# Kernel optimization log

Hardware: AMD Instinct MI355X
Metric: run time of the kernel (lower is better)

The kernel has to match this reference:

```python
import math
import jax, jax.numpy as jnp
import numpy as np

SCALING = 16.0 / 32.0  # alpha / rank


def real_fourier_orthogonal_multiply(c):
    """Vectorized equivalent of the per-frequency Python loop: build a complex
    spectrum from real Fourier coefficients and inverse-rfft along last dim."""
    n = c.shape[-1]
    sqrt_n = math.sqrt(n)
    pair_scale = math.sqrt(n / 2.0)
    max_f = (n - 1) // 2
    work = c.astype(jnp.float32)
    dc = (work[..., 0] * sqrt_n)[..., None].astype(jnp.complex64)
    cos = work[..., 1:1 + 2 * max_f:2] * pair_scale
    sin = work[..., 2:2 + 2 * max_f:2] * pair_scale
    mid = (cos - 1j * sin).astype(jnp.complex64)  # freqs 1..max_f
    parts = [dc, mid]
    if n % 2 == 0:
        parts.append((work[..., -1] * sqrt_n)[..., None].astype(jnp.complex64))
    spectrum = jnp.concatenate(parts, axis=-1)  # [..., n//2+1]
    return jnp.fft.irfft(spectrum, n=n, axis=-1).astype(c.dtype)


def setup_inputs() -> dict:
    key = jax.random.key(0)
    ks = jax.random.split(key, 9)
    B, S, D_in, D_out, R0, R1, E = 4, 2048, 4096, 4096, 32, 8, 3
    x = jax.random.normal(ks[0], (B, S, D_in), dtype=jnp.float32)
    W_base = jax.random.normal(ks[1], (D_out, D_in), dtype=jnp.float32) * 0.02
    b_base = jax.random.normal(ks[2], (D_out,), dtype=jnp.float32) * 0.02
    enc0 = jax.random.normal(ks[3], (R0, D_in), dtype=jnp.float32) * 0.02
    enc1 = jax.random.normal(ks[4], (R1, D_in), dtype=jnp.float32) * 0.02
    coefs0 = jax.random.normal(ks[5], (E, D_out, R0), dtype=jnp.float32) * 0.02
    coefs1 = jax.random.normal(ks[6], (E, D_out, R1), dtype=jnp.float32) * 0.02
    # sparse decoder masks (buffers in the torch module)
    mask0 = jax.random.randint(ks[7], (E, D_out, R0), 0, 2).astype(bool)
    mask1 = jax.random.randint(ks[8], (E, D_out, R1), 0, 2).astype(bool)
    return dict(x=x, W_base=W_base, b_base=b_base, enc0=enc0, enc1=enc1,
                coefs0=coefs0, coefs1=coefs1, mask0=mask0, mask1=mask1)


def reference(x, W_base, b_base, enc0, enc1, coefs0, coefs1, mask0, mask1):
    # base linear
    base = jnp.einsum('bsd,od->bso', x, W_base) + b_base
    # encoder blocks (shared across experts)
    e0 = jnp.einsum('bsd,rd->bsr', x, enc0)  # [B,S,R0]
    e1 = jnp.einsum('bsd,rd->bsr', x, enc1)  # [B,S,R1]
    # masked decoder blocks per expert, summed over blocks
    w0 = coefs0 * mask0.astype(coefs0.dtype)  # [E,O,R0]
    w1 = coefs1 * mask1.astype(coefs1.dtype)  # [E,O,R1]
    decoded = (jnp.einsum('bsr,eor->ebso', e0, w0)
               + jnp.einsum('bsr,eor->ebso', e1, w1))  # [E,B,S,O]
    transformed = real_fourier_orthogonal_multiply(decoded)
    update = transformed.sum(axis=0)  # sum over active experts
    return base + update * SCALING
```

## Files before the change

### kernel.cpp

```cpp
#include <hip/hip_runtime.h>

typedef __attribute__((ext_vector_type(4))) float f32x4;
typedef __attribute__((ext_vector_type(8))) short bf16x8;
typedef __attribute__((ext_vector_type(8))) unsigned short u16x8;

#define GL2LDS(g, l) __builtin_amdgcn_global_load_lds( \
    (const __attribute__((address_space(1))) void*)(g), \
    (__attribute__((address_space(3))) void*)(l), 16, 0, 0)

__device__ __forceinline__ unsigned short f2bf(float x) {
    union { float f; unsigned u; } v; v.f = x;
    unsigned r = (v.u + 0x7FFF + ((v.u >> 16) & 1)) >> 16;
    return (unsigned short)r;
}

__global__ __launch_bounds__(256) void k_prep(const float* __restrict__ c0,
                                              const float* __restrict__ c1,
                                              const int* __restrict__ m0,
                                              const int* __restrict__ m1,
                                              float* __restrict__ Wc,
                                              const float* __restrict__ x,
                                              unsigned short* __restrict__ xb) {
    int b = blockIdx.x;
    if (b < 640) {
        int idx = b * 256 + threadIdx.x;
        if (idx >= 4096 * 40) return;
        int o = idx / 40, c = idx % 40;
        float s = 0.f;
        if (c < 32) {
            #pragma unroll
            for (int e = 0; e < 3; ++e) {
                int i = (e * 4096 + o) * 32 + c;
                s += c0[i] * (m0[i] != 0 ? 1.f : 0.f);
            }
        } else {
            int r = c - 32;
            #pragma unroll
            for (int e = 0; e < 3; ++e) {
                int i = (e * 4096 + o) * 8 + r;
                s += c1[i] * (m1[i] != 0 ? 1.f : 0.f);
            }
        }
        Wc[idx] = s;
    } else {
        int idx = (b - 640) * 256 + threadIdx.x;
        f32x4 f0 = ((const f32x4*)x)[(size_t)idx * 2];
        f32x4 f1 = ((const f32x4*)x)[(size_t)idx * 2 + 1];
        u16x8 o;
        o[0] = f2bf(f0[0]); o[1] = f2bf(f0[1]); o[2] = f2bf(f0[2]); o[3] = f2bf(f0[3]);
        o[4] = f2bf(f1[0]); o[5] = f2bf(f1[1]); o[6] = f2bf(f1[2]); o[7] = f2bf(f1[3]);
        *(u16x8*)(xb + (size_t)idx * 8) = o;
    }
}

__global__ __launch_bounds__(256) void k_gmat(const float* __restrict__ Wc,
                                              float* __restrict__ G) {
    __shared__ float lds[10752];
    int tid = threadIdx.x;
    int t_base = blockIdx.x * 16;
    int f_slot = tid & 15;
    int tg = (tid >> 4) & 3;
    int rg = tid >> 6;
    float acc[4][10];
    #pragma unroll
    for (int a = 0; a < 4; ++a)
        #pragma unroll
        for (int b = 0; b < 10; ++b) acc[a][b] = 0.f;

    for (int ch = 0; ch < 16; ++ch) {
        __syncthreads();
        #pragma unroll
        for (int j = 0; j < 10; ++j) {
            int idx = tid + j * 256;
            int row = idx / 20;
            int v = idx % 20;
            int f = ch * 128 + row;
            f32x4 val = {0.f, 0.f, 0.f, 0.f};
            if (f >= 1) val = *(const f32x4*)(Wc + (2 * f - 1) * 40 + v * 4);
            *(f32x4*)(lds + row * 84 + v * 4) = val;
        }
        __syncthreads();
        #pragma unroll
        for (int j2 = 0; j2 < 8; ++j2) {
            int f_local = f_slot + 16 * j2;
            int f = ch * 128 + f_local;
            float cs[4], sn[4];
            #pragma unroll
            for (int tt = 0; tt < 4; ++tt) {
                int t = t_base + tg * 4 + tt;
                int ph = (f * t) & 4095;
                float rev = (float)ph * (1.0f / 4096.0f);
                cs[tt] = __builtin_amdgcn_cosf(rev);
                sn[tt] = __builtin_amdgcn_sinf(rev);
            }
            const float* Lc = lds + f_local * 84 + rg * 10;
            const float* Ls = Lc + 40;
            #pragma unroll
            for (int rr = 0; rr < 10; ++rr) {
                float wc = Lc[rr], ws = Ls[rr];
                #pragma unroll
                for (int tt = 0; tt < 4; ++tt)
                    acc[tt][rr] += cs[tt] * wc + sn[tt] * ws;
            }
        }
    }
    __syncthreads();
    #pragma unroll
    for (int tt = 0; tt < 4; ++tt)
        #pragma unroll
        for (int rr = 0; rr < 10; ++rr)
            lds[tid * 40 + tt * 10 + rr] = acc[tt][rr];
    __syncthreads();
    for (int oi = tid; oi < 640; oi += 256) {
        int t_local = oi / 40, rc = oi % 40;
        int tg2 = t_local >> 2, tsub = t_local & 3;
        int rg2 = rc / 10, rsub = rc % 10;
        float s = 0.f;
        #pragma unroll
        for (int fs = 0; fs < 16; ++fs)
            s += lds[(fs + tg2 * 16 + rg2 * 64) * 40 + tsub * 10 + rsub];
        int t = t_base + t_local;
        float dc = Wc[rc];
        float ny = Wc[4095 * 40 + rc];
        float sign = (t & 1) ? -1.f : 1.f;
        float g = 0.5f * (0.0220970869120796f * s + (dc + sign * ny) * (1.0f / 64.0f));
        G[t * 40 + rc] = g;
    }
}

__global__ __launch_bounds__(256) void k_wcomb(const float* __restrict__ Wb,
                                               const float* __restrict__ enc0,
                                               const float* __restrict__ enc1,
                                               const float* __restrict__ G,
                                               unsigned short* __restrict__ Wcb) {
    __shared__ float ldsE[40 * 256];
    __shared__ float ldsG[32 * 40];
    int tid = threadIdx.x;
    int d0 = blockIdx.x * 256;
    int t0 = blockIdx.y * 32;
    #pragma unroll
    for (int j = 0; j < 10; ++j) {
        int idx = tid + j * 256;
        int k = idx / 64, v = idx % 64;
        const float* src = (k < 32) ? (enc0 + (size_t)k * 4096) : (enc1 + (size_t)(k - 32) * 4096);
        *(f32x4*)(ldsE + k * 256 + v * 4) = *(const f32x4*)(src + d0 + v * 4);
    }
    #pragma unroll
    for (int j = 0; j < 5; ++j) {
        int idx = tid + j * 256;
        ldsG[idx] = G[(size_t)(t0 + idx / 40) * 40 + (idx % 40)];
    }
    __syncthreads();
    int dg = tid & 31, tg = tid >> 5;
    f32x4 a0[4], a1[4];
    #pragma unroll
    for (int tt = 0; tt < 4; ++tt) { a0[tt] = (f32x4){0,0,0,0}; a1[tt] = (f32x4){0,0,0,0}; }
    #pragma unroll 8
    for (int r = 0; r < 40; ++r) {
        f32x4 e0 = *(const f32x4*)(ldsE + r * 256 + dg * 8);
        f32x4 e1 = *(const f32x4*)(ldsE + r * 256 + dg * 8 + 4);
        #pragma unroll
        for (int tt = 0; tt < 4; ++tt) {
            float g = ldsG[(tg * 4 + tt) * 40 + r];
            a0[tt] += g * e0;
            a1[tt] += g * e1;
        }
    }
    #pragma unroll
    for (int tt = 0; tt < 4; ++tt) {
        int t = t0 + tg * 4 + tt;
        int d = d0 + dg * 8;
        f32x4 w0 = *(const f32x4*)(Wb + (size_t)t * 4096 + d);
        f32x4 w1 = *(const f32x4*)(Wb + (size_t)t * 4096 + d + 4);
        f32x4 r0 = a0[tt] + w0, r1 = a1[tt] + w1;
        u16x8 o;
        o[0] = f2bf(r0[0]); o[1] = f2bf(r0[1]); o[2] = f2bf(r0[2]); o[3] = f2bf(r0[3]);
        o[4] = f2bf(r1[0]); o[5] = f2bf(r1[1]); o[6] = f2bf(r1[2]); o[7] = f2bf(r1[3]);
        *(u16x8*)(Wcb + (size_t)t * 4096 + d) = o;
    }
}

__global__ __launch_bounds__(256) void k_gemm(const unsigned short* __restrict__ A,
                                              const unsigned short* __restrict__ B,
                                              const float* __restrict__ bias,
                                              float* __restrict__ C) {
    __shared__ short As[128 * 64];
    __shared__ short Bs[128 * 64];
    int tid = threadIdx.x;
    int lane = tid & 63, w = tid >> 6;
    int m0 = blockIdx.y * 128, n0 = blockIdx.x * 128;
    int wm = w >> 1, wn = w & 1;
    int lr = lane & 15, q = lane >> 4;

    f32x4 acc[4][4];
    #pragma unroll
    for (int i = 0; i < 4; ++i)
        #pragma unroll
        for (int j = 0; j < 4; ++j) acc[i][j] = (f32x4){0.f, 0.f, 0.f, 0.f};

    int rw = lane >> 3;
    int cg = (lane & 7) ^ rw;
    const unsigned short* Ab = A + (size_t)(m0 + w * 32 + rw) * 4096 + cg * 8;
    const unsigned short* Bb = B + (size_t)(n0 + w * 32 + rw) * 4096 + cg * 8;

    for (int kt = 0; kt < 4096; kt += 64) {
        __syncthreads();
        #pragma unroll
        for (int i = 0; i < 4; ++i) {
            GL2LDS(Ab + (size_t)(i * 8) * 4096 + kt, &As[(w * 32 + i * 8) * 64]);
            GL2LDS(Bb + (size_t)(i * 8) * 4096 + kt, &Bs[(w * 32 + i * 8) * 64]);
        }
        __syncthreads();
        int sw = lr & 7;
        #pragma unroll
        for (int ks = 0; ks < 2; ++ks) {
            bf16x8 af[4], bfr[4];
            #pragma unroll
            for (int i = 0; i < 4; ++i)
                af[i] = *(const bf16x8*)&As[(wm * 64 + i * 16 + lr) * 64 + (((ks * 4 + q) ^ sw) * 8)];
            #pragma unroll
            for (int j = 0; j < 4; ++j)
                bfr[j] = *(const bf16x8*)&Bs[(wn * 64 + j * 16 + lr) * 64 + (((ks * 4 + q) ^ sw) * 8)];
            #pragma unroll
            for (int i = 0; i < 4; ++i)
                #pragma unroll
                for (int j = 0; j < 4; ++j)
                    acc[i][j] = __builtin_amdgcn_mfma_f32_16x16x32_bf16(af[i], bfr[j], acc[i][j], 0, 0, 0);
        }
    }

    float bv[4];
    #pragma unroll
    for (int j = 0; j < 4; ++j) bv[j] = bias[n0 + wn * 64 + j * 16 + lr];
    #pragma unroll
    for (int i = 0; i < 4; ++i) {
        int rbase = m0 + wm * 64 + i * 16 + q * 4;
        #pragma unroll
        for (int r = 0; r < 4; ++r) {
            float* crow = C + (size_t)(rbase + r) * 4096 + n0 + wn * 64 + lr;
            #pragma unroll
            for (int j = 0; j < 4; ++j)
                crow[j * 16] = acc[i][j][r] + bv[j];
        }
    }
}

extern "C" void kernel_launch(void* const* d_in, const int* in_sizes, int n_in,
                              void* d_out, int out_size, void* d_ws, size_t ws_size,
                              hipStream_t stream) {
    const float* x   = (const float*)d_in[0];
    const float* Wb  = (const float*)d_in[1];
    const float* bb  = (const float*)d_in[2];
    const float* e0  = (const float*)d_in[3];
    const float* e1  = (const float*)d_in[4];
    const float* c0  = (const float*)d_in[5];
    const float* c1  = (const float*)d_in[6];
    const int*   m0  = (const int*)d_in[7];
    const int*   m1  = (const int*)d_in[8];
    float* out = (float*)d_out;

    char* ws = (char*)d_ws;
    unsigned short* xb  = (unsigned short*)ws;
    float* Wc           = (float*)(ws + 67108864);
    float* G            = (float*)(ws + 67764224);
    unsigned short* Wcb = (unsigned short*)(ws + 68419584);

    k_prep <<<17024, 256, 0, stream>>>(c0, c1, m0, m1, Wc, x, xb);
    k_gmat <<<256, 256, 0, stream>>>(Wc, G);
    k_wcomb<<<dim3(16, 128), 256, 0, stream>>>(Wb, e0, e1, G, Wcb);
    k_gemm <<<dim3(32, 64), 256, 0, stream>>>(xb, Wcb, bb, out);
}
```

Measured before the change: 705.7 us.

## Use 32x32x16 MFMA in GEMM, spread gmat over more blocks, fix wcomb LDS pattern

The main GEMM switches from 16x16x32 bf16 MFMA tiles to 32x32x16 tiles, with a 2x2 accumulator grid per wave. This halves the LDS fragment loads per MFMA and gives a new output row mapping in the epilogue. k_gmat now handles 8 output rows per block instead of 16 and launches twice as many blocks, to improve occupancy across CUs. k_wcomb reads and writes f32x2 slices strided by 64 columns instead of contiguous 8-float chunks, which is meant to reduce LDS bank conflicts at the cost of narrower global stores.

```diff
diff --git a/kernel.cpp b/kernel.cpp
--- a/kernel.cpp
+++ b/kernel.cpp
@@ -1,6 +1,8 @@
 #include <hip/hip_runtime.h>
 
+typedef __attribute__((ext_vector_type(2))) float f32x2;
 typedef __attribute__((ext_vector_type(4))) float f32x4;
+typedef __attribute__((ext_vector_type(16))) float f32x16;
 typedef __attribute__((ext_vector_type(8))) short bf16x8;
 typedef __attribute__((ext_vector_type(8))) unsigned short u16x8;
 
@@ -57,9 +59,9 @@
                                               float* __restrict__ G) {
     __shared__ float lds[10752];
     int tid = threadIdx.x;
-    int t_base = blockIdx.x * 16;
-    int f_slot = tid & 15;
-    int tg = (tid >> 4) & 3;
+    int t_base = blockIdx.x * 8;
+    int f_slot = tid & 31;
+    int tg = (tid >> 5) & 1;
     int rg = tid >> 6;
     float acc[4][10];
     #pragma unroll
@@ -81,8 +83,8 @@
         }
         __syncthreads();
         #pragma unroll
-        for (int j2 = 0; j2 < 8; ++j2) {
-            int f_local = f_slot + 16 * j2;
+        for (int j2 = 0; j2 < 4; ++j2) {
+            int f_local = f_slot + 32 * j2;
             int f = ch * 128 + f_local;
             float cs[4], sn[4];
             #pragma unroll
@@ -111,14 +113,14 @@
         for (int rr = 0; rr < 10; ++rr)
             lds[tid * 40 + tt * 10 + rr] = acc[tt][rr];
     __syncthreads();
-    for (int oi = tid; oi < 640; oi += 256) {
+    for (int oi = tid; oi < 320; oi += 256) {
         int t_local = oi / 40, rc = oi % 40;
         int tg2 = t_local >> 2, tsub = t_local & 3;
         int rg2 = rc / 10, rsub = rc % 10;
         float s = 0.f;
         #pragma unroll
-        for (int fs = 0; fs < 16; ++fs)
-            s += lds[(fs + tg2 * 16 + rg2 * 64) * 40 + tsub * 10 + rsub];
+        for (int fs = 0; fs < 32; ++fs)
+            s += lds[(fs + tg2 * 32 + rg2 * 64) * 40 + tsub * 10 + rsub];
         int t = t_base + t_local;
         float dc = Wc[rc];
         float ny = Wc[4095 * 40 + rc];
@@ -152,31 +154,36 @@
     }
     __syncthreads();
     int dg = tid & 31, tg = tid >> 5;
-    f32x4 a0[4], a1[4];
-    #pragma unroll
-    for (int tt = 0; tt < 4; ++tt) { a0[tt] = (f32x4){0,0,0,0}; a1[tt] = (f32x4){0,0,0,0}; }
+    f32x2 a[4][4];
+    #pragma unroll
+    for (int s = 0; s < 4; ++s)
+        #pragma unroll
+        for (int tt = 0; tt < 4; ++tt) a[s][tt] = (f32x2){0.f, 0.f};
     #pragma unroll 8
     for (int r = 0; r < 40; ++r) {
-        f32x4 e0 = *(const f32x4*)(ldsE + r * 256 + dg * 8);
-        f32x4 e1 = *(const f32x4*)(ldsE + r * 256 + dg * 8 + 4);
+        f32x2 e[4];
+        #pragma unroll
+        for (int s = 0; s < 4; ++s)
+            e[s] = *(const f32x2*)(ldsE + r * 256 + s * 64 + dg * 2);
         #pragma unroll
         for (int tt = 0; tt < 4; ++tt) {
             float g = ldsG[(tg * 4 + tt) * 40 + r];
-            a0[tt] += g * e0;
-            a1[tt] += g * e1;
+            #pragma unroll
+            for (int s = 0; s < 4; ++s)
+                a[s][tt] += g * e[s];
         }
     }
     #pragma unroll
     for (int tt = 0; tt < 4; ++tt) {
         int t = t0 + tg * 4 + tt;
-        int d = d0 + dg * 8;
-        f32x4 w0 = *(const f32x4*)(Wb + (size_t)t * 4096 + d);
-        f32x4 w1 = *(const f32x4*)(Wb + (size_t)t * 4096 + d + 4);
-        f32x4 r0 = a0[tt] + w0, r1 = a1[tt] + w1;
-        u16x8 o;
-        o[0] = f2bf(r0[0]); o[1] = f2bf(r0[1]); o[2] = f2bf(r0[2]); o[3] = f2bf(r0[3]);
-        o[4] = f2bf(r1[0]); o[5] = f2bf(r1[1]); o[6] = f2bf(r1[2]); o[7] = f2bf(r1[3]);
-        *(u16x8*)(Wcb + (size_t)t * 4096 + d) = o;
+        #pragma unroll
+        for (int s = 0; s < 4; ++s) {
+            int d = d0 + s * 64 + dg * 2;
+            f32x2 wv = *(const f32x2*)(Wb + (size_t)t * 4096 + d);
+            f32x2 rv = a[s][tt] + wv;
+            unsigned short lo = f2bf(rv[0]), hi = f2bf(rv[1]);
+            *(unsigned*)(Wcb + (size_t)t * 4096 + d) = (unsigned)lo | ((unsigned)hi << 16);
+        }
     }
 }
 
@@ -190,19 +197,26 @@
     int lane = tid & 63, w = tid >> 6;
     int m0 = blockIdx.y * 128, n0 = blockIdx.x * 128;
     int wm = w >> 1, wn = w & 1;
-    int lr = lane & 15, q = lane >> 4;
-
-    f32x4 acc[4][4];
-    #pragma unroll
-    for (int i = 0; i < 4; ++i)
-        #pragma unroll
-        for (int j = 0; j < 4; ++j) acc[i][j] = (f32x4){0.f, 0.f, 0.f, 0.f};
+    int col = lane & 31;
+    int hi = lane >> 5;
+    int sw = col & 7;
+
+    f32x16 acc[2][2];
+    #pragma unroll
+    for (int i = 0; i < 2; ++i)
+        #pragma unroll
+        for (int j = 0; j < 2; ++j)
+            #pragma unroll
+            for (int r = 0; r < 16; ++r) acc[i][j][r] = 0.f;
 
     int rw = lane >> 3;
     int cg = (lane & 7) ^ rw;
     const unsigned short* Ab = A + (size_t)(m0 + w * 32 + rw) * 4096 + cg * 8;
     const unsigned short* Bb = B + (size_t)(n0 + w * 32 + rw) * 4096 + cg * 8;
 
+    int aoff0 = (wm * 64 + col) * 64;
+    int boff0 = (wn * 64 + col) * 64;
+
     for (int kt = 0; kt < 4096; kt += 64) {
         __syncthreads();
         #pragma unroll
@@ -211,38 +225,32 @@
             GL2LDS(Bb + (size_t)(i * 8) * 4096 + kt, &Bs[(w * 32 + i * 8) * 64]);
         }
         __syncthreads();
-        int sw = lr & 7;
-        #pragma unroll
-        for (int ks = 0; ks < 2; ++ks) {
-            bf16x8 af[4], bfr[4];
-            #pragma unroll
-            for (int i = 0; i < 4; ++i)
-                af[i] = *(const bf16x8*)&As[(wm * 64 + i * 16 + lr) * 64 + (((ks * 4 + q) ^ sw) * 8)];
-            #pragma unroll
-            for (int j = 0; j < 4; ++j)
-                bfr[j] = *(const bf16x8*)&Bs[(wn * 64 + j * 16 + lr) * 64 + (((ks * 4 + q) ^ sw) * 8)];
-            #pragma unroll
-            for (int i = 0; i < 4; ++i)
-                #pragma unroll
-                for (int j = 0; j < 4; ++j)
-                    acc[i][j] = __builtin_amdgcn_mfma_f32_16x16x32_bf16(af[i], bfr[j], acc[i][j], 0, 0, 0);
-        }
-    }
-
-    float bv[4];
-    #pragma unroll
-    for (int j = 0; j < 4; ++j) bv[j] = bias[n0 + wn * 64 + j * 16 + lr];
-    #pragma unroll
-    for (int i = 0; i < 4; ++i) {
-        int rbase = m0 + wm * 64 + i * 16 + q * 4;
-        #pragma unroll
-        for (int r = 0; r < 4; ++r) {
-            float* crow = C + (size_t)(rbase + r) * 4096 + n0 + wn * 64 + lr;
-            #pragma unroll
-            for (int j = 0; j < 4; ++j)
-                crow[j * 16] = acc[i][j][r] + bv[j];
-        }
-    }
+        #pragma unroll
+        for (int ks = 0; ks < 4; ++ks) {
+            int co = ((ks * 2 + hi) ^ sw) * 8;
+            bf16x8 a0 = *(const bf16x8*)&As[aoff0 + co];
+            bf16x8 a1 = *(const bf16x8*)&As[aoff0 + 32 * 64 + co];
+            bf16x8 b0 = *(const bf16x8*)&Bs[boff0 + co];
+            bf16x8 b1 = *(const bf16x8*)&Bs[boff0 + 32 * 64 + co];
+            acc[0][0] = __builtin_amdgcn_mfma_f32_32x32x16_bf16(a0, b0, acc[0][0], 0, 0, 0);
+            acc[0][1] = __builtin_amdgcn_mfma_f32_32x32x16_bf16(a0, b1, acc[0][1], 0, 0, 0);
+            acc[1][0] = __builtin_amdgcn_mfma_f32_32x32x16_bf16(a1, b0, acc[1][0], 0, 0, 0);
+            acc[1][1] = __builtin_amdgcn_mfma_f32_32x32x16_bf16(a1, b1, acc[1][1], 0, 0, 0);
+        }
+    }
+
+    float bv[2];
+    #pragma unroll
+    for (int j = 0; j < 2; ++j) bv[j] = bias[n0 + wn * 64 + j * 32 + col];
+    #pragma unroll
+    for (int i = 0; i < 2; ++i)
+        #pragma unroll
+        for (int r = 0; r < 16; ++r) {
+            int row = m0 + wm * 64 + i * 32 + (r & 3) + 8 * (r >> 2) + 4 * hi;
+            float* crow = C + (size_t)row * 4096 + n0 + wn * 64 + col;
+            crow[0]  = acc[i][0][r] + bv[0];
+            crow[32] = acc[i][1][r] + bv[1];
+        }
 }
 
 extern "C" void kernel_launch(void* const* d_in, const int* in_sizes, int n_in,
@@ -266,7 +274,7 @@
     unsigned short* Wcb = (unsigned short*)(ws + 68419584);
 
     k_prep <<<17024, 256, 0, stream>>>(c0, c1, m0, m1, Wc, x, xb);
-    k_gmat <<<256, 256, 0, stream>>>(Wc, G);
+    k_gmat <<<512, 256, 0, stream>>>(Wc, G);
     k_wcomb<<<dim3(16, 128), 256, 0, stream>>>(Wb, e0, e1, G, Wcb);
     k_gemm <<<dim3(32, 64), 256, 0, stream>>>(xb, Wcb, bb, out);
 }
```

After: 642.1 us. 9.0% less time.
